# Kernel tuning notes

Measured on AMD Instinct MI355X. Metric: run time of the kernel, lower is better.

## Reference

```python
import jax, jax.numpy as jnp
import numpy as np

N = 50000
E = 625000
D = 128
L = 3
BN_EPS = 1e-5


def setup_inputs() -> dict:
    key = jax.random.key(0)
    ks = jax.random.split(key, 12)
    x = jax.random.normal(ks[0], (N, D), dtype=jnp.float32)
    edge_index = jax.random.randint(ks[1], (2, E), 0, N, dtype=jnp.int64)
    s = 1.0 / np.sqrt(D)
    W1 = jax.random.uniform(ks[2], (L, D, D), jnp.float32, -s, s)
    b1 = jax.random.uniform(ks[3], (L, D), jnp.float32, -s, s)
    W2 = jax.random.uniform(ks[4], (L, D, D), jnp.float32, -s, s)
    b2 = jax.random.uniform(ks[5], (L, D), jnp.float32, -s, s)
    eps = jnp.zeros((L,), jnp.float32)  # GINConv train_eps init 0
    gamma = jnp.ones((L, D), jnp.float32)
    beta = jnp.zeros((L, D), jnp.float32)
    Wl = jax.random.uniform(ks[6], (L, D, D), jnp.float32, -s, s)
    bl = jax.random.uniform(ks[7], (L, D), jnp.float32, -s, s)
    return {"x": x, "edge_index": edge_index, "W1": W1, "b1": b1, "W2": W2,
            "b2": b2, "eps": eps, "gamma": gamma, "beta": beta, "Wl": Wl, "bl": bl}


def reference(x, edge_index, W1, b1, W2, b2, eps, gamma, beta, Wl, bl):
    src, dst = edge_index[0], edge_index[1]
    xs = [x]
    h = x
    for i in range(L):
        # GIN aggregation: sum of neighbor (source) features at target nodes
        agg = jax.ops.segment_sum(h[src], dst, num_segments=N)  # [N, D]
        z = (1.0 + eps[i]) * h + agg
        # MLP: Linear -> ReLU -> Linear
        z = jax.nn.relu(z @ W1[i] + b1[i]) @ W2[i] + b2[i]
        # BatchNorm1d (training mode: batch stats, biased variance)
        mu = jnp.mean(z, axis=0)
        var = jnp.mean((z - mu) ** 2, axis=0)
        z = gamma[i] * (z - mu) * jax.lax.rsqrt(var + BN_EPS) + beta[i]
        if i != 0:
            z = z + xs[-1]
        h = jax.nn.relu(z)
        xs.append(h)
    outs = [xs[i + 1] @ Wl[i] + bl[i] for i in range(L)]
    return jnp.concatenate(outs, axis=-1)  # [N, L*D]
```

## Files before the change

### kernel.cpp

```cpp
#include <hip/hip_runtime.h>
#include <hip/hip_bf16.h>
#include <stdint.h>

#define NN 50000
#define NE 625000
#define DD 128
#define NL 3

typedef __bf16 bf16x8 __attribute__((ext_vector_type(8)));
typedef float f32x4 __attribute__((ext_vector_type(4)));

__device__ __forceinline__ float bflo(uint32_t u) { return __uint_as_float(u << 16); }
__device__ __forceinline__ float bfhi(uint32_t u) { return __uint_as_float(u & 0xffff0000u); }
__device__ __forceinline__ uint16_t f2bf(float f) {
    __hip_bfloat16 h = __float2bfloat16(f);
    return __builtin_bit_cast(uint16_t, h);
}
__device__ __forceinline__ uint32_t pack2(float lo, float hi) {
    return (uint32_t)f2bf(lo) | ((uint32_t)f2bf(hi) << 16);
}

__global__ void k_hist(const int* __restrict__ dstv, int* __restrict__ deg) {
    int e = blockIdx.x * 256 + threadIdx.x;
    if (e < NE) atomicAdd(&deg[dstv[e]], 1);
}

__global__ __launch_bounds__(512) void k_bsum(const int* __restrict__ deg, int* __restrict__ bsum) {
    __shared__ int s[512];
    int i = blockIdx.x * 512 + threadIdx.x;
    int v = (i < NN) ? deg[i] : 0;
    s[threadIdx.x] = v;
    __syncthreads();
    for (int st = 256; st > 0; st >>= 1) {
        if (threadIdx.x < st) s[threadIdx.x] += s[threadIdx.x + st];
        __syncthreads();
    }
    if (threadIdx.x == 0) bsum[blockIdx.x] = s[0];
}

__global__ __launch_bounds__(128) void k_scanbs(const int* __restrict__ bsum, int* __restrict__ bsoff) {
    __shared__ int s[128];
    int t = threadIdx.x;
    int v = (t < 98) ? bsum[t] : 0;
    s[t] = v;
    __syncthreads();
    for (int st = 1; st < 128; st <<= 1) {
        int a = (t >= st) ? s[t - st] : 0;
        __syncthreads();
        s[t] += a;
        __syncthreads();
    }
    if (t < 98) bsoff[t] = s[t] - v;
}

__global__ __launch_bounds__(512) void k_scan2(int* __restrict__ deg_cursor,
                                               const int* __restrict__ bsoff,
                                               int* __restrict__ rowptr) {
    __shared__ int s[512];
    int t = threadIdx.x;
    int i = blockIdx.x * 512 + t;
    int v = (i < NN) ? deg_cursor[i] : 0;
    s[t] = v;
    __syncthreads();
    for (int st = 1; st < 512; st <<= 1) {
        int a = (t >= st) ? s[t - st] : 0;
        __syncthreads();
        s[t] += a;
        __syncthreads();
    }
    if (i < NN) {
        int excl = bsoff[blockIdx.x] + s[t] - v;
        rowptr[i] = excl;
        deg_cursor[i] = excl;
        if (i == NN - 1) rowptr[NN] = excl + v;
    }
}

__global__ void k_fill(const int* __restrict__ srcv, const int* __restrict__ dstv,
                       int* __restrict__ cursor, int* __restrict__ colv) {
    int e = blockIdx.x * 256 + threadIdx.x;
    if (e < NE) {
        int d = dstv[e];
        int p = atomicAdd(&cursor[d], 1);
        colv[p] = srcv[e];
    }
}

__global__ void k_convert_w(const float* __restrict__ W1, const float* __restrict__ W2,
                            const float* __restrict__ Wl, uint16_t* __restrict__ Wb) {
    int id = blockIdx.x * 256 + threadIdx.x;
    if (id >= 9 * 16384) return;
    int m = id >> 14;
    int r = id & 16383;
    int k = r >> 7;
    int col = r & 127;
    const float* src;
    if (m < 3) src = W1 + m * 16384;
    else if (m < 6) src = W2 + (m - 3) * 16384;
    else src = Wl + (m - 6) * 16384;
    float v = src[k * 128 + col];
    Wb[m * 16384 + col * 128 + (k ^ ((col & 7) << 3))] = f2bf(v);
}

__global__ void k_x2bf(const float* __restrict__ x, uint16_t* __restrict__ hb,
                       int* __restrict__ cursor) {
    int id = blockIdx.x * 256 + threadIdx.x;
    if (id < NN) cursor[id] = 0;
    int base = id * 4;
    if (base >= NN * DD) return;
    float4 v = *(const float4*)(x + base);
    uint2 st;
    st.x = pack2(v.x, v.y);
    st.y = pack2(v.z, v.w);
    *(uint2*)(hb + base) = st;
}

__global__ __launch_bounds__(256) void k_agg(const uint16_t* __restrict__ hb,
                                             const int* __restrict__ rowptr,
                                             const int* __restrict__ colv,
                                             const float* __restrict__ epsp, int layer,
                                             uint16_t* __restrict__ zb) {
    int g = (blockIdx.x * 256 + threadIdx.x) >> 4;
    int l16 = threadIdx.x & 15;
    if (g >= NN) return;
    float onepe = 1.0f + epsp[layer];
    int beg = rowptr[g], end = rowptr[g + 1];
    const uint4* hp = (const uint4*)hb;
    float a0 = 0.f, a1 = 0.f, a2 = 0.f, a3 = 0.f, a4 = 0.f, a5 = 0.f, a6 = 0.f, a7 = 0.f;
    int j = beg;
    for (; j + 1 < end; j += 2) {
        int s0 = colv[j];
        int s1 = colv[j + 1];
        uint4 u = hp[(size_t)s0 * 16 + l16];
        uint4 v = hp[(size_t)s1 * 16 + l16];
        a0 += bflo(u.x); a1 += bfhi(u.x); a2 += bflo(u.y); a3 += bfhi(u.y);
        a4 += bflo(u.z); a5 += bfhi(u.z); a6 += bflo(u.w); a7 += bfhi(u.w);
        a0 += bflo(v.x); a1 += bfhi(v.x); a2 += bflo(v.y); a3 += bfhi(v.y);
        a4 += bflo(v.z); a5 += bfhi(v.z); a6 += bflo(v.w); a7 += bfhi(v.w);
    }
    if (j < end) {
        int s0 = colv[j];
        uint4 u = hp[(size_t)s0 * 16 + l16];
        a0 += bflo(u.x); a1 += bfhi(u.x); a2 += bflo(u.y); a3 += bfhi(u.y);
        a4 += bflo(u.z); a5 += bfhi(u.z); a6 += bflo(u.w); a7 += bfhi(u.w);
    }
    uint4 hu = hp[(size_t)g * 16 + l16];
    a0 = fmaf(onepe, bflo(hu.x), a0); a1 = fmaf(onepe, bfhi(hu.x), a1);
    a2 = fmaf(onepe, bflo(hu.y), a2); a3 = fmaf(onepe, bfhi(hu.y), a3);
    a4 = fmaf(onepe, bflo(hu.z), a4); a5 = fmaf(onepe, bfhi(hu.z), a5);
    a6 = fmaf(onepe, bflo(hu.w), a6); a7 = fmaf(onepe, bfhi(hu.w), a7);
    uint4 st;
    st.x = pack2(a0, a1); st.y = pack2(a2, a3);
    st.z = pack2(a4, a5); st.w = pack2(a6, a7);
    ((uint4*)zb)[(size_t)g * 16 + l16] = st;
}

template <int MODE>
__global__ __launch_bounds__(256) void k_gemm(const uint16_t* __restrict__ A,
                                              const uint16_t* __restrict__ Wimg,
                                              const float* __restrict__ bias,
                                              float* __restrict__ bnsum,
                                              void* __restrict__ outp, int ldc, int col_off) {
    __shared__ uint16_t lds[16384];
    int tid = threadIdx.x;
    int wid = tid >> 6, lane = tid & 63;

#pragma unroll
    for (int it = 0; it < 8; ++it) {
        int idx = (it * 256 + tid) * 8;
        bf16x8 v = *(const bf16x8*)(Wimg + idx);
        *(bf16x8*)(&lds[idx]) = v;
    }
    __syncthreads();

    const int brow = blockIdx.x * 128;
    const int m0 = wid * 32;
    const int l15 = lane & 15;
    const int lhi = lane >> 4;

    f32x4 acc[2][8];
    f32x4 zero = {0.f, 0.f, 0.f, 0.f};
#pragma unroll
    for (int m = 0; m < 2; ++m)
#pragma unroll
        for (int n = 0; n < 8; ++n) acc[m][n] = zero;

    const char* Ab = (const char*)A;
#pragma unroll
    for (int kk = 0; kk < 4; ++kk) {
        int kbyte = kk * 64 + (lhi << 4);
        bf16x8 afrag[2];
#pragma unroll
        for (int m = 0; m < 2; ++m) {
            int row = brow + m0 + m * 16 + l15;
            if (row >= NN) row = NN - 1;
            afrag[m] = *(const bf16x8*)(Ab + (size_t)row * 256 + kbyte);
        }
#pragma unroll
        for (int n = 0; n < 8; ++n) {
            int col = n * 16 + l15;
            int addr = col * 256 + (kbyte ^ ((col & 7) << 4));
            bf16x8 bfrag = *(const bf16x8*)((const char*)lds + addr);
            acc[0][n] = __builtin_amdgcn_mfma_f32_16x16x32_bf16(afrag[0], bfrag, acc[0][n], 0, 0, 0);
            acc[1][n] = __builtin_amdgcn_mfma_f32_16x16x32_bf16(afrag[1], bfrag, acc[1][n], 0, 0, 0);
        }
    }

    float bcol[8];
#pragma unroll
    for (int n = 0; n < 8; ++n) bcol[n] = bias[n * 16 + l15];

    float s1[8], s2[8];
#pragma unroll
    for (int n = 0; n < 8; ++n) { s1[n] = 0.f; s2[n] = 0.f; }

#pragma unroll
    for (int m = 0; m < 2; ++m) {
        int rbase = brow + m0 + m * 16 + (lhi << 2);
#pragma unroll
        for (int r = 0; r < 4; ++r) {
            int row = rbase + r;
            bool ok = row < NN;
#pragma unroll
            for (int n = 0; n < 8; ++n) {
                float v = acc[m][n][r] + bcol[n];
                int col = n * 16 + l15;
                if (MODE == 0) {
                    v = fmaxf(v, 0.f);
                    if (ok) ((uint16_t*)outp)[(size_t)row * 128 + col] = f2bf(v);
                } else if (MODE == 1) {
                    if (ok) {
                        ((float*)outp)[(size_t)row * 128 + col] = v;
                        s1[n] += v;
                        s2[n] += v * v;
                    }
                } else {
                    if (ok) ((float*)outp)[(size_t)row * ldc + col_off + col] = v;
                }
            }
        }
    }

    if (MODE == 1) {
        __syncthreads();
        float* ls = (float*)lds;
        ls[tid] = 0.f;
        __syncthreads();
#pragma unroll
        for (int n = 0; n < 8; ++n) {
            float a1 = s1[n] + __shfl_xor(s1[n], 16);
            a1 += __shfl_xor(a1, 32);
            float a2 = s2[n] + __shfl_xor(s2[n], 16);
            a2 += __shfl_xor(a2, 32);
            if (lane < 16) {
                atomicAdd(&ls[n * 16 + lane], a1);
                atomicAdd(&ls[128 + n * 16 + lane], a2);
            }
        }
        __syncthreads();
        atomicAdd(&bnsum[tid], ls[tid]);
    }
}

__global__ void k_bn_fin(const float* __restrict__ bnsum, const float* __restrict__ gamma,
                         const float* __restrict__ beta, int layer, float* __restrict__ bnab) {
    int c = threadIdx.x;
    float mu = bnsum[c] * (1.0f / NN);
    float var = bnsum[128 + c] * (1.0f / NN) - mu * mu;
    float a = gamma[layer * 128 + c] * rsqrtf(var + 1e-5f);
    float b = beta[layer * 128 + c] - mu * a;
    bnab[c] = a;
    bnab[128 + c] = b;
}

__global__ __launch_bounds__(256) void k_apply(const float* __restrict__ z2,
                                               const uint16_t* __restrict__ hin,
                                               const float* __restrict__ bnab, int layer,
                                               uint16_t* __restrict__ hout) {
    int id = blockIdx.x * 256 + threadIdx.x;
    int base = id * 4;
    if (base >= NN * DD) return;
    int c = base & 127;
    float4 z = *(const float4*)(z2 + base);
    float4 av = *(const float4*)(bnab + c);
    float4 bv = *(const float4*)(bnab + 128 + c);
    float v0 = fmaf(av.x, z.x, bv.x);
    float v1 = fmaf(av.y, z.y, bv.y);
    float v2 = fmaf(av.z, z.z, bv.z);
    float v3 = fmaf(av.w, z.w, bv.w);
    if (layer > 0) {
        uint2 h = *(const uint2*)(hin + base);
        v0 += bflo(h.x);
        v1 += bfhi(h.x);
        v2 += bflo(h.y);
        v3 += bfhi(h.y);
    }
    v0 = fmaxf(v0, 0.f);
    v1 = fmaxf(v1, 0.f);
    v2 = fmaxf(v2, 0.f);
    v3 = fmaxf(v3, 0.f);
    uint2 st;
    st.x = pack2(v0, v1);
    st.y = pack2(v2, v3);
    *(uint2*)(hout + base) = st;
}

extern "C" void kernel_launch(void* const* d_in, const int* in_sizes, int n_in,
                              void* d_out, int out_size, void* d_ws, size_t ws_size,
                              hipStream_t stream) {
    const float* x = (const float*)d_in[0];
    const int* ei = (const int*)d_in[1];
    const float* W1 = (const float*)d_in[2];
    const float* b1 = (const float*)d_in[3];
    const float* W2 = (const float*)d_in[4];
    const float* b2 = (const float*)d_in[5];
    const float* epsp = (const float*)d_in[6];
    const float* gamma = (const float*)d_in[7];
    const float* beta = (const float*)d_in[8];
    const float* Wl = (const float*)d_in[9];
    const float* bl = (const float*)d_in[10];
    float* out = (float*)d_out;

    char* w = (char*)d_ws;
    size_t off = 0;
    auto take = [&](size_t b) -> char* {
        char* p = w + off;
        off += (b + 255) & ~(size_t)255;
        return p;
    };
    uint16_t* hbA = (uint16_t*)take((size_t)NN * DD * 2);
    uint16_t* hbB = (uint16_t*)take((size_t)NN * DD * 2);
    uint16_t* zb = (uint16_t*)take((size_t)NN * DD * 2);
    uint16_t* t1b = (uint16_t*)take((size_t)NN * DD * 2);
    float* z2 = (float*)take((size_t)NN * DD * 4);
    int* rowptr = (int*)take((size_t)(NN + 1) * 4);
    int* cursor = (int*)take((size_t)NN * 4);
    int* colv = (int*)take((size_t)NE * 4);
    int* bsum = (int*)take(128 * 4);
    int* bsoff = (int*)take(128 * 4);
    uint16_t* Wb = (uint16_t*)take(9 * 16384 * 2);
    float* bnsum = (float*)take(256 * 4);
    float* bnab = (float*)take(256 * 4);

    const int* srcv = ei;
    const int* dstv = ei + NE;

    k_convert_w<<<(9 * 16384 + 255) / 256, 256, 0, stream>>>(W1, W2, Wl, Wb);
    k_x2bf<<<(NN * DD / 4 + 255) / 256, 256, 0, stream>>>(x, hbA, cursor);

    k_hist<<<(NE + 255) / 256, 256, 0, stream>>>(dstv, cursor);
    k_bsum<<<98, 512, 0, stream>>>(cursor, bsum);
    k_scanbs<<<1, 128, 0, stream>>>(bsum, bsoff);
    k_scan2<<<98, 512, 0, stream>>>(cursor, bsoff, rowptr);
    k_fill<<<(NE + 255) / 256, 256, 0, stream>>>(srcv, dstv, cursor, colv);

    uint16_t* hcur = hbA;
    uint16_t* hnext = hbB;
    const int gemm_blocks = (NN + 127) / 128;
    const int agg_blocks = (NN * 16 + 255) / 256;

    for (int l = 0; l < NL; ++l) {
        k_agg<<<agg_blocks, 256, 0, stream>>>(hcur, rowptr, colv, epsp, l, zb);
        k_gemm<0><<<gemm_blocks, 256, 0, stream>>>(zb, Wb + l * 16384, b1 + l * 128,
                                                   nullptr, t1b, 128, 0);
        hipMemsetAsync(bnsum, 0, 256 * 4, stream);
        k_gemm<1><<<gemm_blocks, 256, 0, stream>>>(t1b, Wb + (3 + l) * 16384, b2 + l * 128,
                                                   bnsum, z2, 128, 0);
        k_bn_fin<<<1, 128, 0, stream>>>(bnsum, gamma, beta, l, bnab);
        k_apply<<<(NN * DD / 4 + 255) / 256, 256, 0, stream>>>(z2, hcur, bnab, l, hnext);
        k_gemm<2><<<gemm_blocks, 256, 0, stream>>>(hnext, Wb + (6 + l) * 16384, bl + l * 128,
                                                   nullptr, out, NL * DD, l * 128);
        uint16_t* t = hcur;
        hcur = hnext;
        hnext = t;
    }
}
```

Before: 313.9 us.

## Batch output GEMMs into one launch and fold BN finalize and memset into kernels

Keeps all three layer activations in separate buffers so the three final projection GEMMs run as a single batched launch at the end. The bnsum memset moves into the aggregation kernel and the BN finalize moves into the apply kernel, removing several small launches per layer. The aggregation loop is also unrolled by four to expose more outstanding gathers. This costs one extra activation buffer, and the BN scale and shift are now recomputed in every apply block.

```diff
diff --git a/kernel.cpp b/kernel.cpp
--- a/kernel.cpp
+++ b/kernel.cpp
@@ -6,6 +6,7 @@
 #define NE 625000
 #define DD 128
 #define NL 3
+#define GB 391
 
 typedef __bf16 bf16x8 __attribute__((ext_vector_type(8)));
 typedef float f32x4 __attribute__((ext_vector_type(4)));
@@ -119,7 +120,9 @@
                                              const int* __restrict__ rowptr,
                                              const int* __restrict__ colv,
                                              const float* __restrict__ epsp, int layer,
-                                             uint16_t* __restrict__ zb) {
+                                             uint16_t* __restrict__ zb,
+                                             float* __restrict__ bnsum) {
+    if (blockIdx.x == 0) bnsum[threadIdx.x] = 0.f;
     int g = (blockIdx.x * 256 + threadIdx.x) >> 4;
     int l16 = threadIdx.x & 15;
     if (g >= NN) return;
@@ -128,17 +131,25 @@
     const uint4* hp = (const uint4*)hb;
     float a0 = 0.f, a1 = 0.f, a2 = 0.f, a3 = 0.f, a4 = 0.f, a5 = 0.f, a6 = 0.f, a7 = 0.f;
     int j = beg;
-    for (; j + 1 < end; j += 2) {
+    for (; j + 3 < end; j += 4) {
         int s0 = colv[j];
         int s1 = colv[j + 1];
-        uint4 u = hp[(size_t)s0 * 16 + l16];
-        uint4 v = hp[(size_t)s1 * 16 + l16];
-        a0 += bflo(u.x); a1 += bfhi(u.x); a2 += bflo(u.y); a3 += bfhi(u.y);
-        a4 += bflo(u.z); a5 += bfhi(u.z); a6 += bflo(u.w); a7 += bfhi(u.w);
-        a0 += bflo(v.x); a1 += bfhi(v.x); a2 += bflo(v.y); a3 += bfhi(v.y);
-        a4 += bflo(v.z); a5 += bfhi(v.z); a6 += bflo(v.w); a7 += bfhi(v.w);
-    }
-    if (j < end) {
+        int s2 = colv[j + 2];
+        int s3 = colv[j + 3];
+        uint4 u0 = hp[(size_t)s0 * 16 + l16];
+        uint4 u1 = hp[(size_t)s1 * 16 + l16];
+        uint4 u2 = hp[(size_t)s2 * 16 + l16];
+        uint4 u3 = hp[(size_t)s3 * 16 + l16];
+        a0 += bflo(u0.x); a1 += bfhi(u0.x); a2 += bflo(u0.y); a3 += bfhi(u0.y);
+        a4 += bflo(u0.z); a5 += bfhi(u0.z); a6 += bflo(u0.w); a7 += bfhi(u0.w);
+        a0 += bflo(u1.x); a1 += bfhi(u1.x); a2 += bflo(u1.y); a3 += bfhi(u1.y);
+        a4 += bflo(u1.z); a5 += bfhi(u1.z); a6 += bflo(u1.w); a7 += bfhi(u1.w);
+        a0 += bflo(u2.x); a1 += bfhi(u2.x); a2 += bflo(u2.y); a3 += bfhi(u2.y);
+        a4 += bflo(u2.z); a5 += bfhi(u2.z); a6 += bflo(u2.w); a7 += bfhi(u2.w);
+        a0 += bflo(u3.x); a1 += bfhi(u3.x); a2 += bflo(u3.y); a3 += bfhi(u3.y);
+        a4 += bflo(u3.z); a5 += bfhi(u3.z); a6 += bflo(u3.w); a7 += bfhi(u3.w);
+    }
+    for (; j < end; ++j) {
         int s0 = colv[j];
         uint4 u = hp[(size_t)s0 * 16 + l16];
         a0 += bflo(u.x); a1 += bfhi(u.x); a2 += bflo(u.y); a3 += bfhi(u.y);
@@ -160,7 +171,7 @@
                                               const uint16_t* __restrict__ Wimg,
                                               const float* __restrict__ bias,
                                               float* __restrict__ bnsum,
-                                              void* __restrict__ outp, int ldc, int col_off) {
+                                              void* __restrict__ outp) {
     __shared__ uint16_t lds[16384];
     int tid = threadIdx.x;
     int wid = tid >> 6, lane = tid & 63;
@@ -228,14 +239,12 @@
                 if (MODE == 0) {
                     v = fmaxf(v, 0.f);
                     if (ok) ((uint16_t*)outp)[(size_t)row * 128 + col] = f2bf(v);
-                } else if (MODE == 1) {
+                } else {
                     if (ok) {
                         ((float*)outp)[(size_t)row * 128 + col] = v;
                         s1[n] += v;
                         s2[n] += v * v;
                     }
-                } else {
-                    if (ok) ((float*)outp)[(size_t)row * ldc + col_off + col] = v;
                 }
             }
         }
@@ -262,28 +271,29 @@
     }
 }
 
-__global__ void k_bn_fin(const float* __restrict__ bnsum, const float* __restrict__ gamma,
-                         const float* __restrict__ beta, int layer, float* __restrict__ bnab) {
-    int c = threadIdx.x;
-    float mu = bnsum[c] * (1.0f / NN);
-    float var = bnsum[128 + c] * (1.0f / NN) - mu * mu;
-    float a = gamma[layer * 128 + c] * rsqrtf(var + 1e-5f);
-    float b = beta[layer * 128 + c] - mu * a;
-    bnab[c] = a;
-    bnab[128 + c] = b;
-}
-
 __global__ __launch_bounds__(256) void k_apply(const float* __restrict__ z2,
                                                const uint16_t* __restrict__ hin,
-                                               const float* __restrict__ bnab, int layer,
+                                               const float* __restrict__ bnsum,
+                                               const float* __restrict__ gamma,
+                                               const float* __restrict__ beta, int layer,
                                                uint16_t* __restrict__ hout) {
-    int id = blockIdx.x * 256 + threadIdx.x;
+    __shared__ float sA[128], sB[128];
+    int tid = threadIdx.x;
+    if (tid < 128) {
+        float mu = bnsum[tid] * (1.0f / NN);
+        float var = bnsum[128 + tid] * (1.0f / NN) - mu * mu;
+        float a = gamma[layer * 128 + tid] * rsqrtf(var + 1e-5f);
+        sA[tid] = a;
+        sB[tid] = beta[layer * 128 + tid] - mu * a;
+    }
+    __syncthreads();
+    int id = blockIdx.x * 256 + tid;
     int base = id * 4;
     if (base >= NN * DD) return;
     int c = base & 127;
     float4 z = *(const float4*)(z2 + base);
-    float4 av = *(const float4*)(bnab + c);
-    float4 bv = *(const float4*)(bnab + 128 + c);
+    float4 av = *(const float4*)(sA + c);
+    float4 bv = *(const float4*)(sB + c);
     float v0 = fmaf(av.x, z.x, bv.x);
     float v1 = fmaf(av.y, z.y, bv.y);
     float v2 = fmaf(av.z, z.z, bv.z);
@@ -303,6 +313,83 @@
     st.x = pack2(v0, v1);
     st.y = pack2(v2, v3);
     *(uint2*)(hout + base) = st;
+}
+
+__global__ __launch_bounds__(256) void k_outgemm(const uint16_t* __restrict__ h1,
+                                                 const uint16_t* __restrict__ h2,
+                                                 const uint16_t* __restrict__ h3,
+                                                 const uint16_t* __restrict__ Wb6,
+                                                 const float* __restrict__ bl,
+                                                 float* __restrict__ out) {
+    __shared__ uint16_t lds[16384];
+    int layer = blockIdx.x / GB;
+    int blk = blockIdx.x - layer * GB;
+    const uint16_t* A = (layer == 0) ? h1 : ((layer == 1) ? h2 : h3);
+    const uint16_t* Wimg = Wb6 + layer * 16384;
+    const float* bias = bl + layer * 128;
+
+    int tid = threadIdx.x;
+    int wid = tid >> 6, lane = tid & 63;
+#pragma unroll
+    for (int it = 0; it < 8; ++it) {
+        int idx = (it * 256 + tid) * 8;
+        bf16x8 v = *(const bf16x8*)(Wimg + idx);
+        *(bf16x8*)(&lds[idx]) = v;
+    }
+    __syncthreads();
+
+    const int brow = blk * 128;
+    const int m0 = wid * 32;
+    const int l15 = lane & 15;
+    const int lhi = lane >> 4;
+
+    f32x4 acc[2][8];
+    f32x4 zero = {0.f, 0.f, 0.f, 0.f};
+#pragma unroll
+    for (int m = 0; m < 2; ++m)
+#pragma unroll
+        for (int n = 0; n < 8; ++n) acc[m][n] = zero;
+
+    const char* Ab = (const char*)A;
+#pragma unroll
+    for (int kk = 0; kk < 4; ++kk) {
+        int kbyte = kk * 64 + (lhi << 4);
+        bf16x8 afrag[2];
+#pragma unroll
+        for (int m = 0; m < 2; ++m) {
+            int row = brow + m0 + m * 16 + l15;
+            if (row >= NN) row = NN - 1;
+            afrag[m] = *(const bf16x8*)(Ab + (size_t)row * 256 + kbyte);
+        }
+#pragma unroll
+        for (int n = 0; n < 8; ++n) {
+            int col = n * 16 + l15;
+            int addr = col * 256 + (kbyte ^ ((col & 7) << 4));
+            bf16x8 bfrag = *(const bf16x8*)((const char*)lds + addr);
+            acc[0][n] = __builtin_amdgcn_mfma_f32_16x16x32_bf16(afrag[0], bfrag, acc[0][n], 0, 0, 0);
+            acc[1][n] = __builtin_amdgcn_mfma_f32_16x16x32_bf16(afrag[1], bfrag, acc[1][n], 0, 0, 0);
+        }
+    }
+
+    float bcol[8];
+#pragma unroll
+    for (int n = 0; n < 8; ++n) bcol[n] = bias[n * 16 + l15];
+
+#pragma unroll
+    for (int m = 0; m < 2; ++m) {
+        int rbase = brow + m0 + m * 16 + (lhi << 2);
+#pragma unroll
+        for (int r = 0; r < 4; ++r) {
+            int row = rbase + r;
+            if (row < NN) {
+#pragma unroll
+                for (int n = 0; n < 8; ++n) {
+                    float v = acc[m][n][r] + bcol[n];
+                    out[(size_t)row * (NL * DD) + layer * 128 + n * 16 + l15] = v;
+                }
+            }
+        }
+    }
 }
 
 extern "C" void kernel_launch(void* const* d_in, const int* in_sizes, int n_in,
@@ -328,8 +415,8 @@
         off += (b + 255) & ~(size_t)255;
         return p;
     };
-    uint16_t* hbA = (uint16_t*)take((size_t)NN * DD * 2);
-    uint16_t* hbB = (uint16_t*)take((size_t)NN * DD * 2);
+    uint16_t* hb[4];
+    for (int i = 0; i < 4; ++i) hb[i] = (uint16_t*)take((size_t)NN * DD * 2);
     uint16_t* zb = (uint16_t*)take((size_t)NN * DD * 2);
     uint16_t* t1b = (uint16_t*)take((size_t)NN * DD * 2);
     float* z2 = (float*)take((size_t)NN * DD * 4);
@@ -340,13 +427,12 @@
     int* bsoff = (int*)take(128 * 4);
     uint16_t* Wb = (uint16_t*)take(9 * 16384 * 2);
     float* bnsum = (float*)take(256 * 4);
-    float* bnab = (float*)take(256 * 4);
 
     const int* srcv = ei;
     const int* dstv = ei + NE;
 
     k_convert_w<<<(9 * 16384 + 255) / 256, 256, 0, stream>>>(W1, W2, Wl, Wb);
-    k_x2bf<<<(NN * DD / 4 + 255) / 256, 256, 0, stream>>>(x, hbA, cursor);
+    k_x2bf<<<(NN * DD / 4 + 255) / 256, 256, 0, stream>>>(x, hb[0], cursor);
 
     k_hist<<<(NE + 255) / 256, 256, 0, stream>>>(dstv, cursor);
     k_bsum<<<98, 512, 0, stream>>>(cursor, bsum);
@@ -354,24 +440,14 @@
     k_scan2<<<98, 512, 0, stream>>>(cursor, bsoff, rowptr);
     k_fill<<<(NE + 255) / 256, 256, 0, stream>>>(srcv, dstv, cursor, colv);
 
-    uint16_t* hcur = hbA;
-    uint16_t* hnext = hbB;
-    const int gemm_blocks = (NN + 127) / 128;
     const int agg_blocks = (NN * 16 + 255) / 256;
 
     for (int l = 0; l < NL; ++l) {
-        k_agg<<<agg_blocks, 256, 0, stream>>>(hcur, rowptr, colv, epsp, l, zb);
-        k_gemm<0><<<gemm_blocks, 256, 0, stream>>>(zb, Wb + l * 16384, b1 + l * 128,
-                                                   nullptr, t1b, 128, 0);
-        hipMemsetAsync(bnsum, 0, 256 * 4, stream);
-        k_gemm<1><<<gemm_blocks, 256, 0, stream>>>(t1b, Wb + (3 + l) * 16384, b2 + l * 128,
-                                                   bnsum, z2, 128, 0);
-        k_bn_fin<<<1, 128, 0, stream>>>(bnsum, gamma, beta, l, bnab);
-        k_apply<<<(NN * DD / 4 + 255) / 256, 256, 0, stream>>>(z2, hcur, bnab, l, hnext);
-        k_gemm<2><<<gemm_blocks, 256, 0, stream>>>(hnext, Wb + (6 + l) * 16384, bl + l * 128,
-                                                   nullptr, out, NL * DD, l * 128);
-        uint16_t* t = hcur;
-        hcur = hnext;
-        hnext = t;
-    }
-}
+        k_agg<<<agg_blocks, 256, 0, stream>>>(hb[l], rowptr, colv, epsp, l, zb, bnsum);
+        k_gemm<0><<<GB, 256, 0, stream>>>(zb, Wb + l * 16384, b1 + l * 128, nullptr, t1b);
+        k_gemm<1><<<GB, 256, 0, stream>>>(t1b, Wb + (3 + l) * 16384, b2 + l * 128, bnsum, z2);
+        k_apply<<<(NN * DD / 4 + 255) / 256, 256, 0, stream>>>(z2, hb[l], bnsum, gamma, beta,
+                                                               l, hb[l + 1]);
+    }
+    k_outgemm<<<NL * GB, 256, 0, stream>>>(hb[1], hb[2], hb[3], Wb + 6 * 16384, bl, out);
+}
```

Result: faster. 290.9 us (-7.3%).
